# Kernel optimization log

Measured on AMD Instinct MI355X. Metric: run time of the kernel, lower is better.

Reference implementation:

```python
import jax, jax.numpy as jnp
import numpy as np


def setup_inputs() -> dict:
    key = jax.random.key(0)
    ks = jax.random.split(key, 6)
    B, H, W, Cin, Cout, wdim = 8, 64, 64, 512, 512, 512
    return {
        "x": jax.random.normal(ks[0], (B, H, W, Cin), jnp.float32),
        "w": jax.random.normal(ks[1], (B, wdim), jnp.float32),
        "noise": jax.random.normal(ks[2], (B, H, W, 1), jnp.float32),
        "style_weight": jax.random.normal(ks[3], (wdim, Cin), jnp.float32),
        "style_bias": jnp.ones((Cin,), jnp.float32),
        "conv_weight": jax.random.normal(ks[4], (3, 3, Cin, Cout), jnp.float32),
        "scale_noise": 0.1 * jax.random.normal(ks[5], (1, 1, 1, Cout), jnp.float32),
        "bias": jax.random.normal(jax.random.fold_in(key, 7), (Cout,), jnp.float32),
    }


def reference(x, w, noise, style_weight, style_bias, conv_weight, scale_noise, bias):
    wdim = style_weight.shape[0]
    kh, kw, cin, cout = conv_weight.shape
    # Equalized-LR fully connected to_style (gain=1, lr_mult=1, bias init ones,
    # activation=True -> leaky_relu(0.2) with sqrt(2) gain, StyleGAN2 convention).
    s = w @ (style_weight * (1.0 / np.sqrt(wdim))) + style_bias  # [B, Cin]
    s = jax.nn.leaky_relu(s, 0.2) * np.sqrt(2.0).astype(np.float32)
    # Modulated conv (demodulated). Equalized-LR weight scale 1/sqrt(fan_in).
    wk = conv_weight * (1.0 / np.sqrt(kh * kw * cin))  # [3,3,Cin,Cout]
    # demod[b,o] = rsqrt(sum_{h,w,i} (wk[h,w,i,o]*s[b,i])^2 + eps)
    d = jax.lax.rsqrt(jnp.einsum('hwio,bi->bo', wk * wk, s * s) + 1e-8)  # [B,Cout]
    xm = x * s[:, None, None, :]  # modulate inputs instead of per-sample weights
    y = jax.lax.conv_general_dilated(
        xm, wk, window_strides=(1, 1), padding='SAME',
        dimension_numbers=('NHWC', 'HWIO', 'NHWC'))
    y = y * d[:, None, None, :]
    # noise scale-add + bias + leaky-relu (the fused tail in StyleGAN2 kernels)
    y = y + scale_noise * noise + bias
    return jax.nn.leaky_relu(y, 0.2)
```

## Files before the change

kernel.cpp:

```cpp
#include <hip/hip_runtime.h>
#include <hip/hip_bf16.h>
#include <stdint.h>


typedef __attribute__((ext_vector_type(8))) __bf16 bf16x8;
typedef __attribute__((ext_vector_type(16))) float f32x16;

__device__ __forceinline__ float bf2f(ushort u) {
    union { uint32_t i; float f; } v; v.i = (uint32_t)u << 16; return v.f;
}
__device__ __forceinline__ ushort f2bf(float f) {
    union { float f; uint32_t i; } v; v.f = f;
    uint32_t r = v.i + 0x7fffu + ((v.i >> 16) & 1u);
    return (ushort)(r >> 16);
}
__device__ __forceinline__ int sniff_f32(const void* sb) {
    return ((const uint32_t*)sb)[0] == 0x3F800000u;
}
__device__ __forceinline__ float lda(const void* p, int idx, int isf) {
    return isf ? ((const float*)p)[idx] : bf2f(((const ushort*)p)[idx]);
}

union U16x8 { uint4 v; ushort u[8]; };

#define INV_SQRT_WDIM 0.04419417382415922f
#define SQRT2         1.4142135623730951f
#define WSCALE        0.014731391274719739f

__global__ void k_style_part(const void* __restrict__ w, const void* __restrict__ sw,
                             const void* __restrict__ sb, float* __restrict__ part) {
    int isf = sniff_f32(sb);
    int b = blockIdx.x >> 3, ds = blockIdx.x & 7;
    int i = threadIdx.x;
    __shared__ float wrow[64];
    if (i < 64) wrow[i] = lda(w, b * 512 + ds * 64 + i, isf);
    __syncthreads();
    float acc = 0.f;
    if (isf) {
        const float* p = (const float*)sw + (size_t)ds * 64 * 512;
#pragma unroll 8
        for (int d = 0; d < 64; ++d) acc += wrow[d] * p[d * 512 + i];
    } else {
        const ushort* p = (const ushort*)sw + (size_t)ds * 64 * 512;
#pragma unroll 8
        for (int d = 0; d < 64; ++d) acc += wrow[d] * bf2f(p[d * 512 + i]);
    }
    part[(b * 8 + ds) * 512 + i] = acc;
}

__device__ __forceinline__ float style_s(const float* __restrict__ spart,
                                         const void* __restrict__ sb,
                                         int b, int i, int isf) {
    float a = 0.f;
#pragma unroll
    for (int ds = 0; ds < 8; ++ds) a += spart[(b * 8 + ds) * 512 + i];
    float s = a * INV_SQRT_WDIM + lda(sb, i, isf);
    return (s > 0.f ? s : 0.2f * s) * SQRT2;
}

__global__ void k_prep(const void* __restrict__ cw, const void* __restrict__ x,
                       const float* __restrict__ spart, const void* __restrict__ sb,
                       ushort* __restrict__ wkt2, ushort* __restrict__ xmp2,
                       float* __restrict__ part) {
    int isf = sniff_f32(sb);
    int bid = blockIdx.x;
    int tid = threadIdx.x;
    __shared__ ushort smw[8][512];
    __shared__ float sv[512];
    __shared__ float s2[4096];
    __shared__ float red[2048];

    if (bid < 576) {
        int t = bid / 64, ckg = bid % 64;
#pragma unroll
        for (int r = 0; r < 16; ++r) {
            int l = r * 256 + tid;
            int j = l >> 9, o = l & 511;
            float v = lda(cw, (size_t)(t * 512 + ckg * 8 + j) * 512 + o, isf);
            smw[j][o] = f2bf(v * WSCALE);
        }
        __syncthreads();
#pragma unroll
        for (int r = 0; r < 2; ++r) {
            int o = r * 256 + tid;
            U16x8 pk;
#pragma unroll
            for (int j = 0; j < 8; ++j) pk.u[j] = smw[j][o];
            *(uint4*)(wkt2 + ((size_t)(t * 64 + ckg) * 512 + o) * 8) = pk.v;
        }
        return;
    }
    if (bid < 1104) {
        int pr = bid - 576;
        int b = pr / 66, yp = pr % 66;
        ushort* xb2 = xmp2 + (size_t)b * 2230272;
        uint4 z = {0u, 0u, 0u, 0u};
        if (yp == 0 || yp == 65) {
            for (int l = tid; l < 4224; l += 256) {
                int h = l / 132, cc = l - h * 132;
                *(uint4*)(xb2 + (size_t)(h * 66 + yp) * 1056 + cc * 8) = z;
            }
            return;
        }
        for (int i = tid; i < 512; i += 256) sv[i] = style_s(spart, sb, b, i, isf);
        __syncthreads();
        int y = yp - 1;
#pragma unroll
        for (int r = 0; r < 8; ++r) {
            int u = r * 256 + tid;
            int col = (u & 63) + 1, h = u >> 6;
            ushort* op = xb2 + ((size_t)(h * 66 + yp) * 66 + col) * 16;
            U16x8 o0_, o1_;
            if (isf) {
                const float* xin = (const float*)x
                    + (((size_t)(b * 64 + y)) * 64 + (col - 1)) * 512 + h * 16;
                float4 f0 = *(const float4*)(xin + 0);
                float4 f1 = *(const float4*)(xin + 4);
                float4 f2 = *(const float4*)(xin + 8);
                float4 f3 = *(const float4*)(xin + 12);
                const float* sp = sv + h * 16;
                o0_.u[0] = f2bf(f0.x * sp[0]);  o0_.u[1] = f2bf(f0.y * sp[1]);
                o0_.u[2] = f2bf(f0.z * sp[2]);  o0_.u[3] = f2bf(f0.w * sp[3]);
                o0_.u[4] = f2bf(f1.x * sp[4]);  o0_.u[5] = f2bf(f1.y * sp[5]);
                o0_.u[6] = f2bf(f1.z * sp[6]);  o0_.u[7] = f2bf(f1.w * sp[7]);
                o1_.u[0] = f2bf(f2.x * sp[8]);  o1_.u[1] = f2bf(f2.y * sp[9]);
                o1_.u[2] = f2bf(f2.z * sp[10]); o1_.u[3] = f2bf(f2.w * sp[11]);
                o1_.u[4] = f2bf(f3.x * sp[12]); o1_.u[5] = f2bf(f3.y * sp[13]);
                o1_.u[6] = f2bf(f3.z * sp[14]); o1_.u[7] = f2bf(f3.w * sp[15]);
            } else {
                const ushort* xin = (const ushort*)x
                    + (((size_t)(b * 64 + y)) * 64 + (col - 1)) * 512 + h * 16;
                U16x8 i0, i1;
                i0.v = *(const uint4*)(xin);
                i1.v = *(const uint4*)(xin + 8);
                const float* sp = sv + h * 16;
#pragma unroll
                for (int j = 0; j < 8; ++j) o0_.u[j] = f2bf(bf2f(i0.u[j]) * sp[j]);
#pragma unroll
                for (int j = 0; j < 8; ++j) o1_.u[j] = f2bf(bf2f(i1.u[j]) * sp[8 + j]);
            }
            *(uint4*)(op) = o0_.v;
            *(uint4*)(op + 8) = o1_.v;
        }
        if (tid < 64) {
            int h = tid & 31, side = tid >> 5;
            ushort* op = xb2 + ((size_t)(h * 66 + yp) * 66 + side * 65) * 16;
            *(uint4*)(op) = z;
            *(uint4*)(op + 8) = z;
        }
        return;
    }
    {
        int q2 = bid - 1104;
        int t = q2 / 8, ob = q2 % 8;
#pragma unroll
        for (int j = 0; j < 16; ++j) {
            int idx = j * 256 + tid;
            int bb = idx >> 9, i = idx & 511;
            float scv = style_s(spart, sb, bb, i, isf);
            s2[idx] = scv * scv;
        }
        __syncthreads();
        int q = tid >> 6, ol = tid & 63;
        int o = ob * 64 + ol;
        float accd[8] = {0, 0, 0, 0, 0, 0, 0, 0};
        for (int ii = 0; ii < 128; ++ii) {
            int i = q * 128 + ii;
            float wf = lda(cw, (size_t)(t * 512 + i) * 512 + o, isf) * WSCALE;
            float w2 = wf * wf;
#pragma unroll
            for (int bb = 0; bb < 8; ++bb) accd[bb] += w2 * s2[bb * 512 + i];
        }
#pragma unroll
        for (int bb = 0; bb < 8; ++bb) red[(ol * 8 + bb) * 4 + q] = accd[bb];
        __syncthreads();
#pragma unroll
        for (int p = 0; p < 2; ++p) {
            int u = tid * 2 + p;
            int ol2 = u >> 3, b2 = u & 7;
            float sum = red[u * 4 + 0] + red[u * 4 + 1] + red[u * 4 + 2] + red[u * 4 + 3];
            part[(b2 * 9 + t) * 512 + ob * 64 + ol2] = sum;
        }
    }
}

#define GLL(gp, lp) __builtin_amdgcn_global_load_lds( \
    (const __attribute__((address_space(1))) void*)(gp), \
    (__attribute__((address_space(3))) void*)(lp), 16, 0, 0)

__launch_bounds__(256, 2)
__global__ void k_conv(const ushort* __restrict__ xmp2, const ushort* __restrict__ wkt2,
                       const float* __restrict__ part, const void* __restrict__ noise,
                       const void* __restrict__ snoise, const void* __restrict__ bias_,
                       const void* __restrict__ sb, void* __restrict__ out) {
    __shared__ ushort Ah[2][6336];
    int isf = sniff_f32(sb);
    int id = blockIdx.x;
    int ct = id & 3;
    int rt = (id >> 2) & 15;
    int b  = id >> 6;
    int y0 = rt * 4, o0 = ct * 128;
    int tid = threadIdx.x;
    int lane = tid & 63, wv = tid >> 6;
    int wr = wv >> 1, wc = wv & 1;
    int lm = lane & 31, kh = lane >> 5;
    const ushort* xb2 = xmp2 + (size_t)b * 2230272;
    const ushort* wB = wkt2 + kh * 4096 + (size_t)(o0 + wc * 64 + lm) * 8;

    auto stageA = [&](int hp, int buf) {
        char* dst = (char*)Ah[buf];
#pragma unroll
        for (int it = 0; it < 3; ++it) {
            int L = it * 256 + tid;
            int hr = L / 132, rem = L - hr * 132;
            GLL(xb2 + (size_t)(hp * 66 + y0 + hr) * 1056 + rem * 8, dst + L * 16);
        }
        if (tid < 24) {
            int L = 768 + tid;
            int rem = L - 660;
            GLL(xb2 + (size_t)(hp * 66 + y0 + 5) * 1056 + rem * 8, dst + L * 16);
        }
    };
    auto loadB = [&](int t, int h, bf16x8 (&d)[2]) {
        const ushort* p = wB + (size_t)t * 262144 + h * 8192;
        d[0] = *(const bf16x8*)(p);
        d[1] = *(const bf16x8*)(p + 256);
    };

    f32x16 acc[4][2] = {};
    bf16x8 b0[2], b1[2], b2[2];

    stageA(0, 0);
    loadB(0, 0, b0);
    loadB(1, 0, b1);
    loadB(2, 0, b2);
    __syncthreads();

#pragma unroll 1
    for (int h = 0; h < 32; ++h) {
        const char* AhC = (const char*)Ah[h & 1];
        auto tap = [&](int t, const bf16x8 (&bf)[2]) {
            int dy = t / 3 - 1, dx = t % 3 - 1;
            bf16x8 afr[4];
#pragma unroll
            for (int am = 0; am < 4; ++am)
                afr[am] = *(const bf16x8*)(AhC
                    + (wr * 2 + (am >> 1) + dy + 1) * 2112
                    + ((am & 1) * 32 + lm + dx + 1) * 32 + kh * 16);
#pragma unroll
            for (int am = 0; am < 4; ++am)
#pragma unroll
                for (int bn = 0; bn < 2; ++bn)
                    acc[am][bn] = __builtin_amdgcn_mfma_f32_32x32x16_bf16(
                        afr[am], bf[bn], acc[am][bn], 0, 0, 0);
        };
        tap(0, b0); loadB(3, h, b0);
        if (h < 31) stageA(h + 1, (h + 1) & 1);
        tap(1, b1); loadB(4, h, b1);
        tap(2, b2); loadB(5, h, b2);
        tap(3, b0); loadB(6, h, b0);
        tap(4, b1); loadB(7, h, b1);
        tap(5, b2); loadB(8, h, b2);
        tap(6, b0); if (h < 31) loadB(0, h + 1, b0);
        tap(7, b1); if (h < 31) loadB(1, h + 1, b1);
        tap(8, b2); if (h < 31) loadB(2, h + 1, b2);
        if (h < 31) __syncthreads();
    }

    float dv[2], snv[2], bv[2];
#pragma unroll
    for (int bn = 0; bn < 2; ++bn) {
        int o = o0 + wc * 64 + bn * 32 + lm;
        float a = 1e-8f;
#pragma unroll
        for (int t = 0; t < 9; ++t) a += part[(b * 9 + t) * 512 + o];
        dv[bn] = rsqrtf(a);
        snv[bn] = lda(snoise, o, isf);
        bv[bn] = lda(bias_, o, isf);
    }
#pragma unroll
    for (int am = 0; am < 4; ++am) {
#pragma unroll
        for (int reg = 0; reg < 16; ++reg) {
            int crow = 4 * kh + (reg & 3) + 8 * (reg >> 2);
            int yy = y0 + wr * 2 + (am >> 1);
            int xx = (am & 1) * 32 + crow;
            float nz = lda(noise, (b * 64 + yy) * 64 + xx, isf);
            size_t obase = ((size_t)(b * 64 + yy) * 64 + xx) * 512;
            if (isf) {
                float* of = (float*)out;
#pragma unroll
                for (int bn = 0; bn < 2; ++bn) {
                    float v = acc[am][bn][reg] * dv[bn] + snv[bn] * nz + bv[bn];
                    v = v > 0.f ? v : 0.2f * v;
                    of[obase + o0 + wc * 64 + bn * 32 + lm] = v;
                }
            } else {
                ushort* ob = (ushort*)out;
#pragma unroll
                for (int bn = 0; bn < 2; ++bn) {
                    float v = acc[am][bn][reg] * dv[bn] + snv[bn] * nz + bv[bn];
                    v = v > 0.f ? v : 0.2f * v;
                    ob[obase + o0 + wc * 64 + bn * 32 + lm] = f2bf(v);
                }
            }
        }
    }
}

extern "C" void kernel_launch(void* const* d_in, const int* in_sizes, int n_in,
                              void* d_out, int out_size, void* d_ws, size_t ws_size,
                              hipStream_t stream) {
    const void* x     = d_in[0];
    const void* w     = d_in[1];
    const void* noise = d_in[2];
    const void* sw    = d_in[3];
    const void* sb    = d_in[4];
    const void* cw    = d_in[5];
    const void* sn    = d_in[6];
    const void* bias  = d_in[7];

    char* ws = (char*)d_ws;
    ushort* xmp2  = (ushort*)(ws);
    ushort* wkt2  = (ushort*)(ws + 35684352);
    float*  part  = (float*)(ws + 40435712);
    float*  spart = (float*)(ws + 40583168);
    (void)in_sizes; (void)n_in; (void)out_size; (void)ws_size;

    hipLaunchKernelGGL(k_style_part, dim3(64),   dim3(512), 0, stream, w, sw, sb, spart);
    hipLaunchKernelGGL(k_prep,       dim3(1176), dim3(256), 0, stream,
                       cw, x, spart, sb, wkt2, xmp2, part);
    hipLaunchKernelGGL(k_conv,       dim3(512),  dim3(256), 0, stream,
                       xmp2, wkt2, part, noise, sn, bias, sb, d_out);
}
```

Measured before the change: 306.8 us.

## Double-buffer A fragments in conv loop and transpose modulated input through LDS

The main conv loop now loads the A-operand LDS fragments for the next tap into an alternate register set before issuing MFMAs for the current tap, and raises wave priority around the MFMA block. The aim is to hide LDS read latency behind matrix work. The prep kernel's modulation path now stages converted data through a swizzled LDS buffer, so that both global reads and writes of the padded channel-blocked layout are coalesced. Shared arrays are merged into a single pool. In exchange this adds more VGPR pressure and extra barriers in prep.

```diff
diff --git a/kernel.cpp b/kernel.cpp
--- a/kernel.cpp
+++ b/kernel.cpp
@@ -65,12 +65,10 @@
     int isf = sniff_f32(sb);
     int bid = blockIdx.x;
     int tid = threadIdx.x;
-    __shared__ ushort smw[8][512];
-    __shared__ float sv[512];
-    __shared__ float s2[4096];
-    __shared__ float red[2048];
+    __shared__ __align__(16) char pool[34816];
 
     if (bid < 576) {
+        ushort (*smw)[512] = (ushort (*)[512])pool;
         int t = bid / 64, ckg = bid % 64;
 #pragma unroll
         for (int r = 0; r < 16; ++r) {
@@ -91,6 +89,8 @@
         return;
     }
     if (bid < 1104) {
+        float* sv = (float*)pool;
+        ushort* tr = (ushort*)(pool + 2048);
         int pr = bid - 576;
         int b = pr / 66, yp = pr % 66;
         ushort* xb2 = xmp2 + (size_t)b * 2230272;
@@ -103,54 +103,72 @@
             return;
         }
         for (int i = tid; i < 512; i += 256) sv[i] = style_s(spart, sb, b, i, isf);
-        __syncthreads();
-        int y = yp - 1;
-#pragma unroll
-        for (int r = 0; r < 8; ++r) {
-            int u = r * 256 + tid;
-            int col = (u & 63) + 1, h = u >> 6;
-            ushort* op = xb2 + ((size_t)(h * 66 + yp) * 66 + col) * 16;
-            U16x8 o0_, o1_;
-            if (isf) {
-                const float* xin = (const float*)x
-                    + (((size_t)(b * 64 + y)) * 64 + (col - 1)) * 512 + h * 16;
-                float4 f0 = *(const float4*)(xin + 0);
-                float4 f1 = *(const float4*)(xin + 4);
-                float4 f2 = *(const float4*)(xin + 8);
-                float4 f3 = *(const float4*)(xin + 12);
-                const float* sp = sv + h * 16;
-                o0_.u[0] = f2bf(f0.x * sp[0]);  o0_.u[1] = f2bf(f0.y * sp[1]);
-                o0_.u[2] = f2bf(f0.z * sp[2]);  o0_.u[3] = f2bf(f0.w * sp[3]);
-                o0_.u[4] = f2bf(f1.x * sp[4]);  o0_.u[5] = f2bf(f1.y * sp[5]);
-                o0_.u[6] = f2bf(f1.z * sp[6]);  o0_.u[7] = f2bf(f1.w * sp[7]);
-                o1_.u[0] = f2bf(f2.x * sp[8]);  o1_.u[1] = f2bf(f2.y * sp[9]);
-                o1_.u[2] = f2bf(f2.z * sp[10]); o1_.u[3] = f2bf(f2.w * sp[11]);
-                o1_.u[4] = f2bf(f3.x * sp[12]); o1_.u[5] = f2bf(f3.y * sp[13]);
-                o1_.u[6] = f2bf(f3.z * sp[14]); o1_.u[7] = f2bf(f3.w * sp[15]);
-            } else {
-                const ushort* xin = (const ushort*)x
-                    + (((size_t)(b * 64 + y)) * 64 + (col - 1)) * 512 + h * 16;
-                U16x8 i0, i1;
-                i0.v = *(const uint4*)(xin);
-                i1.v = *(const uint4*)(xin + 8);
-                const float* sp = sv + h * 16;
-#pragma unroll
-                for (int j = 0; j < 8; ++j) o0_.u[j] = f2bf(bf2f(i0.u[j]) * sp[j]);
-#pragma unroll
-                for (int j = 0; j < 8; ++j) o1_.u[j] = f2bf(bf2f(i1.u[j]) * sp[8 + j]);
-            }
-            *(uint4*)(op) = o0_.v;
-            *(uint4*)(op + 8) = o1_.v;
-        }
         if (tid < 64) {
             int h = tid & 31, side = tid >> 5;
             ushort* op = xb2 + ((size_t)(h * 66 + yp) * 66 + side * 65) * 16;
             *(uint4*)(op) = z;
             *(uint4*)(op + 8) = z;
         }
+        int y = yp - 1;
+        __syncthreads();
+#pragma unroll 1
+        for (int p = 0; p < 2; ++p) {
+            if (p) __syncthreads();
+            int c0 = p * 32;
+#pragma unroll
+            for (int r = 0; r < 4; ++r) {
+                int u = r * 256 + tid;
+                int hg = u & 31, col = u >> 5;
+                U16x8 o0_, o1_;
+                const float* sp = sv + hg * 16;
+                if (isf) {
+                    const float* xin = (const float*)x
+                        + (((size_t)(b * 64 + y)) * 64 + c0 + col) * 512 + hg * 16;
+                    float4 f0 = *(const float4*)(xin + 0);
+                    float4 f1 = *(const float4*)(xin + 4);
+                    float4 f2 = *(const float4*)(xin + 8);
+                    float4 f3 = *(const float4*)(xin + 12);
+                    o0_.u[0] = f2bf(f0.x * sp[0]);  o0_.u[1] = f2bf(f0.y * sp[1]);
+                    o0_.u[2] = f2bf(f0.z * sp[2]);  o0_.u[3] = f2bf(f0.w * sp[3]);
+                    o0_.u[4] = f2bf(f1.x * sp[4]);  o0_.u[5] = f2bf(f1.y * sp[5]);
+                    o0_.u[6] = f2bf(f1.z * sp[6]);  o0_.u[7] = f2bf(f1.w * sp[7]);
+                    o1_.u[0] = f2bf(f2.x * sp[8]);  o1_.u[1] = f2bf(f2.y * sp[9]);
+                    o1_.u[2] = f2bf(f2.z * sp[10]); o1_.u[3] = f2bf(f2.w * sp[11]);
+                    o1_.u[4] = f2bf(f3.x * sp[12]); o1_.u[5] = f2bf(f3.y * sp[13]);
+                    o1_.u[6] = f2bf(f3.z * sp[14]); o1_.u[7] = f2bf(f3.w * sp[15]);
+                } else {
+                    const ushort* xin = (const ushort*)x
+                        + (((size_t)(b * 64 + y)) * 64 + c0 + col) * 512 + hg * 16;
+                    U16x8 i0, i1;
+                    i0.v = *(const uint4*)(xin);
+                    i1.v = *(const uint4*)(xin + 8);
+#pragma unroll
+                    for (int j = 0; j < 8; ++j) o0_.u[j] = f2bf(bf2f(i0.u[j]) * sp[j]);
+#pragma unroll
+                    for (int j = 0; j < 8; ++j) o1_.u[j] = f2bf(bf2f(i1.u[j]) * sp[8 + j]);
+                }
+                int cs = col ^ (hg & 7);
+                *(uint4*)(tr + ((hg * 2 + 0) * 32 + cs) * 8) = o0_.v;
+                *(uint4*)(tr + ((hg * 2 + 1) * 32 + cs) * 8) = o1_.v;
+            }
+            __syncthreads();
+#pragma unroll
+            for (int r = 0; r < 4; ++r) {
+                int v = r * 256 + tid;
+                int col = v & 31, hg = v >> 5;
+                int cs = col ^ (hg & 7);
+                uint4 a0 = *(const uint4*)(tr + ((hg * 2 + 0) * 32 + cs) * 8);
+                uint4 a1 = *(const uint4*)(tr + ((hg * 2 + 1) * 32 + cs) * 8);
+                ushort* op = xb2 + ((size_t)(hg * 66 + yp) * 66 + (c0 + col + 1)) * 16;
+                *(uint4*)(op) = a0;
+                *(uint4*)(op + 8) = a1;
+            }
+        }
         return;
     }
     {
+        float* s2 = (float*)pool;
+        float* red = (float*)(pool + 16384);
         int q2 = bid - 1104;
         int t = q2 / 8, ob = q2 % 8;
 #pragma unroll
@@ -239,31 +257,36 @@
 #pragma unroll 1
     for (int h = 0; h < 32; ++h) {
         const char* AhC = (const char*)Ah[h & 1];
-        auto tap = [&](int t, const bf16x8 (&bf)[2]) {
+        bf16x8 afA[4], afB[4];
+        auto ldA = [&](int t, bf16x8 (&af)[4]) {
             int dy = t / 3 - 1, dx = t % 3 - 1;
-            bf16x8 afr[4];
 #pragma unroll
             for (int am = 0; am < 4; ++am)
-                afr[am] = *(const bf16x8*)(AhC
+                af[am] = *(const bf16x8*)(AhC
                     + (wr * 2 + (am >> 1) + dy + 1) * 2112
                     + ((am & 1) * 32 + lm + dx + 1) * 32 + kh * 16);
+        };
+        auto mm = [&](const bf16x8 (&af)[4], const bf16x8 (&bf)[2]) {
+            __builtin_amdgcn_s_setprio(1);
 #pragma unroll
             for (int am = 0; am < 4; ++am)
 #pragma unroll
                 for (int bn = 0; bn < 2; ++bn)
                     acc[am][bn] = __builtin_amdgcn_mfma_f32_32x32x16_bf16(
-                        afr[am], bf[bn], acc[am][bn], 0, 0, 0);
+                        af[am], bf[bn], acc[am][bn], 0, 0, 0);
+            __builtin_amdgcn_s_setprio(0);
         };
-        tap(0, b0); loadB(3, h, b0);
+        ldA(0, afA);
+        ldA(1, afB); mm(afA, b0); loadB(3, h, b0);
         if (h < 31) stageA(h + 1, (h + 1) & 1);
-        tap(1, b1); loadB(4, h, b1);
-        tap(2, b2); loadB(5, h, b2);
-        tap(3, b0); loadB(6, h, b0);
-        tap(4, b1); loadB(7, h, b1);
-        tap(5, b2); loadB(8, h, b2);
-        tap(6, b0); if (h < 31) loadB(0, h + 1, b0);
-        tap(7, b1); if (h < 31) loadB(1, h + 1, b1);
-        tap(8, b2); if (h < 31) loadB(2, h + 1, b2);
+        ldA(2, afA); mm(afB, b1); loadB(4, h, b1);
+        ldA(3, afB); mm(afA, b2); loadB(5, h, b2);
+        ldA(4, afA); mm(afB, b0); loadB(6, h, b0);
+        ldA(5, afB); mm(afA, b1); loadB(7, h, b1);
+        ldA(6, afA); mm(afB, b2); loadB(8, h, b2);
+        ldA(7, afB); mm(afA, b0); if (h < 31) loadB(0, h + 1, b0);
+        ldA(8, afA); mm(afB, b1); if (h < 31) loadB(1, h + 1, b1);
+        mm(afA, b2);              if (h < 31) loadB(2, h + 1, b2);
         if (h < 31) __syncthreads();
     }
 
```

After: 299.8 us. -2.3%, faster.
